# Performance work log

Hardware: AMD Instinct MI355X
Metric: run time of the kernel (lower is better)

## Reference

```python
import jax, jax.numpy as jnp
import numpy as np

SEQ = 2048
D_MODEL = 2048
N_HEAD = 16
D_QK = 128
D_V = 128


def setup_inputs() -> dict:
    key = jax.random.key(0)
    ks = jax.random.split(key, 5)
    return {
        "x": jax.random.normal(ks[0], (SEQ, D_MODEL), dtype=jnp.float32),
        "q": jax.random.normal(ks[1], (N_HEAD, D_MODEL, D_QK), dtype=jnp.float32),
        "k": jax.random.normal(ks[2], (N_HEAD, D_MODEL, D_QK), dtype=jnp.float32),
        "v": jax.random.normal(ks[3], (N_HEAD, D_MODEL, D_V), dtype=jnp.float32),
        "o": jax.random.normal(ks[4], (N_HEAD, D_V, D_MODEL), dtype=jnp.float32),
        "theta_factor": jnp.asarray(10000.0, dtype=jnp.float32),
    }


def _rope_embed(x, theta_factor, d_qk):
    # x: [n_head, seq, d_qk]; faithful to source: rate is LINEAR in theta_factor
    seq = x.shape[1]
    d_rope = d_qk // 2
    rate = theta_factor * (-jnp.arange(d_rope, dtype=x.dtype) / d_rope)  # [d_rope]
    pos = jnp.arange(seq, dtype=x.dtype)                                 # [seq]
    rot = pos[:, None] * rate[None, :]                                   # [seq, d_rope]
    sin, cos = jnp.sin(rot), jnp.cos(rot)
    x1, x2 = x[..., :d_rope], x[..., d_rope:]
    y = jnp.concatenate([cos * x1 - sin * x2, sin * x1 + cos * x2], axis=-1)
    return y / d_qk ** 0.25  # qk_layer_norm is None path


def reference(x, q, k, v, o, theta_factor):
    seq, d_model = x.shape
    n_head, _, d_qk = q.shape
    d_v = v.shape[2]
    scale = 1.0 / jnp.sqrt(jnp.asarray(n_head * d_v * d_model, dtype=x.dtype))
    # causal mask: (tril - 1) * 1e9, as in source
    mask = (jnp.tril(jnp.ones((seq, seq), dtype=x.dtype)) - 1.0) * 1e9
    # per-head projections (vmapped heads expressed as einsum over h)
    rq = _rope_embed(jnp.einsum('sd,hde->hse', x, q), theta_factor, d_qk)
    rk = _rope_embed(jnp.einsum('sd,hde->hse', x, k), theta_factor, d_qk)
    vs = jnp.einsum('sd,hdv->hsv', x, v)
    scores = jnp.einsum('hse,hte->hst', rq, rk) + mask  # [h, s, s]
    w = jax.nn.softmax(scores, axis=-1)
    y = jnp.einsum('hst,htv->hsv', w, vs)
    z = jnp.einsum('hsv,hvd->sd', y, o)
    return z * scale
```

## Files before the change

kernel.cpp:

```cpp
#include <hip/hip_runtime.h>
#include <math.h>


typedef _Float16 half_t;
typedef __attribute__((ext_vector_type(8))) _Float16 half8;
typedef __attribute__((ext_vector_type(4))) float f32x4;

#define SEQ   2048
#define DM    2048
#define NHEAD 16

__device__ __forceinline__ f32x4 mfma16(half8 a, half8 b, f32x4 c) {
  return __builtin_amdgcn_mfma_f32_16x16x32_f16(a, b, c, 0, 0, 0);
}

__device__ __forceinline__ void gll16(const half_t* g, half_t* l) {
  __builtin_amdgcn_global_load_lds(
      (const __attribute__((address_space(1))) unsigned int*)g,
      (__attribute__((address_space(3))) unsigned int*)l, 16, 0, 0);
}

template <int CTRL>
__device__ __forceinline__ float dppf(float v) {
  int r = __builtin_amdgcn_mov_dpp(__builtin_bit_cast(int, v), CTRL, 0xF, 0xF,
                                   true);
  return __builtin_bit_cast(float, r);
}
__device__ __forceinline__ float red16_max(float v) {
  v = fmaxf(v, dppf<0xB1>(v));
  v = fmaxf(v, dppf<0x4E>(v));
  v = fmaxf(v, dppf<0x141>(v));
  v = fmaxf(v, dppf<0x140>(v));
  return v;
}
__device__ __forceinline__ float red16_sum(float v) {
  v += dppf<0xB1>(v);
  v += dppf<0x4E>(v);
  v += dppf<0x141>(v);
  v += dppf<0x140>(v);
  return v;
}

__global__ __launch_bounds__(256)
void k_split4(const float* __restrict__ in, half_t* __restrict__ hi,
              half_t* __restrict__ lo, int n4) {
  int i = blockIdx.x * 256 + threadIdx.x;
  if (i >= n4) return;
  float4 v = ((const float4*)in)[i];
  union { half_t h[4]; uint2 u; } H, L;
  H.h[0] = (half_t)v.x; H.h[1] = (half_t)v.y;
  H.h[2] = (half_t)v.z; H.h[3] = (half_t)v.w;
  L.h[0] = (half_t)(v.x - (float)H.h[0]);
  L.h[1] = (half_t)(v.y - (float)H.h[1]);
  L.h[2] = (half_t)(v.z - (float)H.h[2]);
  L.h[3] = (half_t)(v.w - (float)H.h[3]);
  *(uint2*)&hi[(size_t)i * 4] = H.u;
  *(uint2*)&lo[(size_t)i * 4] = L.u;
}

__global__ __launch_bounds__(256)
void k_transpose(const float* __restrict__ in, half_t* __restrict__ hi,
                 half_t* __restrict__ lo, int R, int C) {
  __shared__ float tile[32][33];
  size_t bo = (size_t)blockIdx.z * R * C;
  int c0 = blockIdx.x * 32, r0 = blockIdx.y * 32;
  int tx = threadIdx.x & 31, ty = threadIdx.x >> 5;
#pragma unroll
  for (int i = 0; i < 32; i += 8)
    tile[ty + i][tx] = in[bo + (size_t)(r0 + ty + i) * C + c0 + tx];
  __syncthreads();
#pragma unroll
  for (int i = 0; i < 32; i += 8) {
    float v = tile[tx][ty + i];
    half_t h = (half_t)v;
    size_t oidx = bo + (size_t)(c0 + ty + i) * R + r0 + tx;
    hi[oidx] = h;
    if (lo) lo[oidx] = (half_t)(v - (float)h);
  }
}


__global__ __launch_bounds__(256, 2)
void k_proj(const half_t* __restrict__ Xh, const half_t* __restrict__ Xl,
            const half_t* __restrict__ WTh, const half_t* __restrict__ WTl,
            float* __restrict__ Craw) {
  __shared__ __align__(16) half_t sAh[128 * 64], sAl[128 * 64];
  __shared__ __align__(16) half_t sBh[128 * 64], sBl[128 * 64];
  int y = blockIdx.y;
  int m0 = blockIdx.x * 128;
  const half_t* wth = WTh + (size_t)y * 128 * DM;
  const half_t* wtl = WTl + (size_t)y * 128 * DM;
  int lane = threadIdx.x & 63, wave = threadIdx.x >> 6;
  int l15 = lane & 15, quad = lane >> 4;
  int wm = wave >> 1, wn = wave & 1;

  f32x4 acc[4][4];
#pragma unroll
  for (int a = 0; a < 4; ++a)
#pragma unroll
    for (int b = 0; b < 4; ++b) acc[a][b] = (f32x4)0.0f;

  for (int kt = 0; kt < DM / 64; ++kt) {
    int k0 = kt * 64;
#pragma unroll
    for (int i = 0; i < 4; ++i) {
      int c = wave * 4 + i;
      int g = c * 64 + lane;
      int row = g >> 3;
      int lc = (g & 7) ^ (row & 7);
      size_t ro = (size_t)row * DM + k0 + lc * 8;
      gll16(Xh + (size_t)m0 * DM + ro, sAh + c * 512);
      gll16(Xl + (size_t)m0 * DM + ro, sAl + c * 512);
      gll16(wth + ro, sBh + c * 512);
      gll16(wtl + ro, sBl + c * 512);
    }
    __syncthreads();
#pragma unroll
    for (int kk = 0; kk < 2; ++kk) {
      half8 ah[4], al[4], bh[4], bl[4];
#pragma unroll
      for (int t = 0; t < 4; ++t) {
        int ar = wm * 64 + t * 16 + l15;
        int br = wn * 64 + t * 16 + l15;
        int ao = ar * 64 + (((kk * 4 + quad) ^ (ar & 7)) * 8);
        int bo = br * 64 + (((kk * 4 + quad) ^ (br & 7)) * 8);
        ah[t] = *(const half8*)&sAh[ao];
        al[t] = *(const half8*)&sAl[ao];
        bh[t] = *(const half8*)&sBh[bo];
        bl[t] = *(const half8*)&sBl[bo];
      }
#pragma unroll
      for (int im = 0; im < 4; ++im)
#pragma unroll
        for (int in = 0; in < 4; ++in) {
          acc[im][in] = mfma16(ah[im], bh[in], acc[im][in]);
          acc[im][in] = mfma16(ah[im], bl[in], acc[im][in]);
          acc[im][in] = mfma16(al[im], bh[in], acc[im][in]);
        }
    }
    __syncthreads();
  }
  float* cb = Craw + (size_t)y * SEQ * 128;
#pragma unroll
  for (int im = 0; im < 4; ++im)
#pragma unroll
    for (int in = 0; in < 4; ++in)
#pragma unroll
      for (int r = 0; r < 4; ++r) {
        int row = m0 + wm * 64 + im * 16 + quad * 4 + r;
        int col = wn * 64 + in * 16 + l15;
        cb[(size_t)row * 128 + col] = acc[im][in][r];
      }
}

__global__ __launch_bounds__(256)
void k_rope(const float* __restrict__ Craw, half_t* __restrict__ Rh,
            half_t* __restrict__ Rl, const float* __restrict__ thetap) {
  int e = threadIdx.x & 63, sl = threadIdx.x >> 6;
  int s = blockIdx.x * 4 + sl;
  float th = thetap[0];
  float rate = th * (-(float)e * (1.0f / 64.0f));
  float rot = (float)s * rate;
  double rev = (double)rot * 0.15915494309189535;
  double fr = rev - rint(rev);
  float thr = (float)(fr * 6.283185307179586);
  float sn = sinf(thr), cs = cosf(thr);
  const float inv4 = 0.2973017787506803f;
  float csn = cs * inv4, snn = sn * inv4;
#pragma unroll 4
  for (int y = 0; y < 32; ++y) {
    size_t base = ((size_t)y * SEQ + s) * 128;
    float x1 = Craw[base + e];
    float x2 = Craw[base + 64 + e];
    float y1 = csn * x1 - snn * x2;
    float y2 = snn * x1 + csn * x2;
    half_t h1 = (half_t)y1, h2 = (half_t)y2;
    Rh[base + e] = h1;       Rl[base + e] = (half_t)(y1 - (float)h1);
    Rh[base + 64 + e] = h2;  Rl[base + 64 + e] = (half_t)(y2 - (float)h2);
  }
}

template <int HALF_OUT>
__global__ __launch_bounds__(256)
void k_gemm1(const half_t* __restrict__ A, const half_t* __restrict__ B,
             void* __restrict__ Cv, float scale) {
  __shared__ __align__(16) half_t sA[128 * 64], sB[128 * 64];
  int am0 = blockIdx.y * 128, bn0 = blockIdx.x * 128;
  int lane = threadIdx.x & 63, wave = threadIdx.x >> 6;
  int l15 = lane & 15, quad = lane >> 4;
  int wm = wave >> 1, wn = wave & 1;

  f32x4 acc[4][4];
#pragma unroll
  for (int a = 0; a < 4; ++a)
#pragma unroll
    for (int b = 0; b < 4; ++b) acc[a][b] = (f32x4)0.0f;

  for (int kt = 0; kt < DM / 64; ++kt) {
    int k0 = kt * 64;
#pragma unroll
    for (int i = 0; i < 4; ++i) {
      int c = wave * 4 + i;
      int g = c * 64 + lane;
      int row = g >> 3;
      int lc = (g & 7) ^ (row & 7);
      size_t ro = (size_t)row * 2048 + k0 + lc * 8;
      gll16(A + (size_t)am0 * 2048 + ro, sA + c * 512);
      gll16(B + (size_t)bn0 * 2048 + ro, sB + c * 512);
    }
    __syncthreads();
#pragma unroll
    for (int kk = 0; kk < 2; ++kk) {
      half8 ah[4], bh[4];
#pragma unroll
      for (int t = 0; t < 4; ++t) {
        int ar = wm * 64 + t * 16 + l15;
        int br = wn * 64 + t * 16 + l15;
        ah[t] = *(const half8*)&sA[ar * 64 + (((kk * 4 + quad) ^ (ar & 7)) * 8)];
        bh[t] = *(const half8*)&sB[br * 64 + (((kk * 4 + quad) ^ (br & 7)) * 8)];
      }
#pragma unroll
      for (int im = 0; im < 4; ++im)
#pragma unroll
        for (int in = 0; in < 4; ++in)
          acc[im][in] = mfma16(ah[im], bh[in], acc[im][in]);
    }
    __syncthreads();
  }
#pragma unroll
  for (int im = 0; im < 4; ++im)
#pragma unroll
    for (int in = 0; in < 4; ++in)
#pragma unroll
      for (int r = 0; r < 4; ++r) {
        int row = am0 + wm * 64 + im * 16 + quad * 4 + r;
        int col = bn0 + wn * 64 + in * 16 + l15;
        if (HALF_OUT)
          ((half_t*)Cv)[(size_t)row * 2048 + col] = (half_t)(acc[im][in][r] * scale);
        else
          ((float*)Cv)[(size_t)row * 2048 + col] = acc[im][in][r] * scale;
      }
}

__global__ __launch_bounds__(256, 2)
void k_flash(const half_t* __restrict__ Rh, const half_t* __restrict__ Rl,
             const half_t* __restrict__ VST, half_t* __restrict__ Ybig) {
  int idx = blockIdx.x;
  int h = idx & 15;
  int qt = (idx < 256) ? (31 - (idx >> 4)) : ((idx - 256) >> 4);
  int lane = threadIdx.x & 63, wave = threadIdx.x >> 6;
  int l15 = lane & 15, quad = lane >> 4;

  const half_t* RQh = Rh + (size_t)h * SEQ * 128;
  const half_t* RQl = Rl + (size_t)h * SEQ * 128;
  const half_t* RKh = Rh + (size_t)(NHEAD + h) * SEQ * 128;
  const half_t* RKl = Rl + (size_t)(NHEAD + h) * SEQ * 128;
  const half_t* Vt  = VST + (size_t)h * 128 * SEQ;

  __shared__ __align__(16) half_t sKh[64 * 128];
  __shared__ __align__(16) half_t sKl[64 * 128];
  __shared__ __align__(16) half_t sVt[128 * 64];
  __shared__ __align__(16) half_t sP[64 * 72];

  int q0 = qt * 64;

  half8 qh[4], ql[4];
#pragma unroll
  for (int kk = 0; kk < 4; ++kk) {
    size_t ad = (size_t)(q0 + wave * 16 + l15) * 128 + kk * 32 + quad * 8;
    qh[kk] = *(const half8*)&RQh[ad];
    ql[kk] = *(const half8*)&RQl[ad];
  }

  float m_st[4], l_st[4];
  f32x4 oacc[8];
#pragma unroll
  for (int r = 0; r < 4; ++r) { m_st[r] = -INFINITY; l_st[r] = 0.0f; }
#pragma unroll
  for (int iv = 0; iv < 8; ++iv) oacc[iv] = (f32x4)0.0f;

  int nkb = qt + 1;
  for (int kb = 0; kb < nkb; ++kb) {
    int t0 = kb * 64;
#pragma unroll
    for (int i = 0; i < 4; ++i) {
      int c = wave * 4 + i;
      int rk = c * 4 + (lane >> 4);
      int ck = (lane & 15) ^ (rk & 15);
      gll16(RKh + (size_t)(t0 + rk) * 128 + ck * 8, sKh + c * 512);
      gll16(RKl + (size_t)(t0 + rk) * 128 + ck * 8, sKl + c * 512);
      int rv = c * 8 + (lane >> 3);
      int cv = (lane & 7) ^ (rv & 7);
      gll16(Vt + (size_t)rv * SEQ + t0 + cv * 8, sVt + c * 512);
    }
    __syncthreads();

    f32x4 sacc[4];
#pragma unroll
    for (int in = 0; in < 4; ++in) sacc[in] = (f32x4)0.0f;
#pragma unroll
    for (int kk = 0; kk < 4; ++kk)
#pragma unroll
      for (int in = 0; in < 4; ++in) {
        int bo = (in * 16 + l15) * 128 + (((kk * 4 + quad) ^ l15) * 8);
        half8 bh = *(const half8*)&sKh[bo];
        half8 bl = *(const half8*)&sKl[bo];
        sacc[in] = mfma16(qh[kk], bh, sacc[in]);
        sacc[in] = mfma16(qh[kk], bl, sacc[in]);
        sacc[in] = mfma16(ql[kk], bh, sacc[in]);
      }
    if (kb == qt) {
#pragma unroll
      for (int in = 0; in < 4; ++in)
#pragma unroll
        for (int r = 0; r < 4; ++r)
          if (in * 16 + l15 > wave * 16 + quad * 4 + r) sacc[in][r] = -1e30f;
    }
    float alpha[4];
#pragma unroll
    for (int r = 0; r < 4; ++r) {
      float mx = fmaxf(fmaxf(sacc[0][r], sacc[1][r]),
                       fmaxf(sacc[2][r], sacc[3][r]));
      mx = red16_max(mx);
      float mnew = fmaxf(m_st[r], mx);
      alpha[r] = __expf(m_st[r] - mnew);
      float sum = 0.0f;
#pragma unroll
      for (int in = 0; in < 4; ++in) {
        float p = __expf(sacc[in][r] - mnew);
        sacc[in][r] = p;
        sum += p;
      }
      sum = red16_sum(sum);
      l_st[r] = l_st[r] * alpha[r] + sum;
      m_st[r] = mnew;
    }
#pragma unroll
    for (int in = 0; in < 4; ++in)
#pragma unroll
      for (int r = 0; r < 4; ++r)
        sP[(wave * 16 + quad * 4 + r) * 72 + in * 16 + l15] =
            (half_t)sacc[in][r];
#pragma unroll
    for (int iv = 0; iv < 8; ++iv)
#pragma unroll
      for (int r = 0; r < 4; ++r) oacc[iv][r] *= alpha[r];

#pragma unroll
    for (int kk2 = 0; kk2 < 2; ++kk2) {
      half8 pa =
          *(const half8*)&sP[(wave * 16 + l15) * 72 + kk2 * 32 + quad * 8];
#pragma unroll
      for (int iv = 0; iv < 8; ++iv) {
        half8 vb = *(const half8*)&sVt[(iv * 16 + l15) * 64 +
                                       (((kk2 * 4 + quad) ^ (l15 & 7)) * 8)];
        oacc[iv] = mfma16(pa, vb, oacc[iv]);
      }
    }
    __syncthreads();
  }
  float invl[4];
#pragma unroll
  for (int r = 0; r < 4; ++r) invl[r] = 1.0f / l_st[r];
#pragma unroll
  for (int iv = 0; iv < 8; ++iv)
#pragma unroll
    for (int r = 0; r < 4; ++r) {
      int row = q0 + wave * 16 + quad * 4 + r;
      int col = h * 128 + iv * 16 + l15;
      Ybig[(size_t)row * 2048 + col] = (half_t)(oacc[iv][r] * invl[r]);
    }
}

extern "C" void kernel_launch(void* const* d_in, const int* in_sizes, int n_in,
                              void* d_out, int out_size, void* d_ws,
                              size_t ws_size, hipStream_t stream) {
  const float* x = (const float*)d_in[0];
  const float* q = (const float*)d_in[1];
  const float* k = (const float*)d_in[2];
  const float* v = (const float*)d_in[3];
  const float* o = (const float*)d_in[4];
  const float* theta = (const float*)d_in[5];
  float* out = (float*)d_out;

  char* ws = (char*)d_ws;
  const size_t HB = (size_t)2048 * 2048 * 2;
  half_t* Xh  = (half_t*)(ws);
  half_t* Xl  = (half_t*)(ws + HB);
  half_t* WTh = (half_t*)(ws + 2 * HB);
  half_t* WTl = (half_t*)(ws + 4 * HB);
  half_t* VhT = (half_t*)(ws + 6 * HB);
  half_t* OT  = (half_t*)(ws + 7 * HB);
  float*  Craw = (float*)(ws + 8 * HB);
  half_t* Rh = WTh;
  half_t* Rl = WTl;
  half_t* VST  = (half_t*)(ws + 8 * HB);
  half_t* Ybig = (half_t*)(ws + 9 * HB);

  k_split4<<<4096, 256, 0, stream>>>(x, Xh, Xl, (2048 * 2048) / 4);
  k_transpose<<<dim3(4, 64, 16), 256, 0, stream>>>(q, WTh, WTl, 2048, 128);
  k_transpose<<<dim3(4, 64, 16), 256, 0, stream>>>(
      k, WTh + (size_t)16 * 128 * 2048, WTl + (size_t)16 * 128 * 2048, 2048, 128);
  k_transpose<<<dim3(4, 64, 16), 256, 0, stream>>>(v, VhT, nullptr, 2048, 128);
  k_transpose<<<dim3(64, 64, 1), 256, 0, stream>>>(o, OT, nullptr, 2048, 2048);
  k_proj<<<dim3(16, 32), 256, 0, stream>>>(Xh, Xl, WTh, WTl, Craw);
  k_rope<<<512, 256, 0, stream>>>(Craw, Rh, Rl, theta);
  k_gemm1<1><<<dim3(16, 16), 256, 0, stream>>>(VhT, Xh, VST, 1.0f);
  k_flash<<<512, 256, 0, stream>>>(Rh, Rl, VST, Ybig);
  k_gemm1<0><<<dim3(16, 16), 256, 0, stream>>>(Ybig, OT, out, 1.0f / 2048.0f);
}
```

Before: 380.9 us.

## Merge preprocessing kernels, fuse RoPE into projection epilogue, halve gemm M tile

Five preprocessing launches (split, four transposes) are merged into one k_pre kernel, which also precomputes a sin/cos table. RoPE moves into the k_proj epilogue: accumulators are staged through LDS and the rotated hi/lo fp16 results are written directly, so the fp32 Craw intermediate round trip and the separate rope launch go away. k_gemm1 switches to 64x128 tiles to double the block count for the V and output GEMMs. This trades more LDS traffic and extra barriers in the projection epilogue, plus a rearranged workspace, for less global memory traffic and launch overhead.

New measurement: 354.7 us. 6.9% less time.

```diff
diff --git a/kernel.cpp b/kernel.cpp
--- a/kernel.cpp
+++ b/kernel.cpp
@@ -41,51 +41,91 @@
   return v;
 }
 
-__global__ __launch_bounds__(256)
-void k_split4(const float* __restrict__ in, half_t* __restrict__ hi,
-              half_t* __restrict__ lo, int n4) {
-  int i = blockIdx.x * 256 + threadIdx.x;
-  if (i >= n4) return;
-  float4 v = ((const float4*)in)[i];
-  union { half_t h[4]; uint2 u; } H, L;
-  H.h[0] = (half_t)v.x; H.h[1] = (half_t)v.y;
-  H.h[2] = (half_t)v.z; H.h[3] = (half_t)v.w;
-  L.h[0] = (half_t)(v.x - (float)H.h[0]);
-  L.h[1] = (half_t)(v.y - (float)H.h[1]);
-  L.h[2] = (half_t)(v.z - (float)H.h[2]);
-  L.h[3] = (half_t)(v.w - (float)H.h[3]);
-  *(uint2*)&hi[(size_t)i * 4] = H.u;
-  *(uint2*)&lo[(size_t)i * 4] = L.u;
-}
-
-__global__ __launch_bounds__(256)
-void k_transpose(const float* __restrict__ in, half_t* __restrict__ hi,
-                 half_t* __restrict__ lo, int R, int C) {
-  __shared__ float tile[32][33];
-  size_t bo = (size_t)blockIdx.z * R * C;
-  int c0 = blockIdx.x * 32, r0 = blockIdx.y * 32;
-  int tx = threadIdx.x & 31, ty = threadIdx.x >> 5;
+__device__ __forceinline__ void tpose32(const float* __restrict__ in,
+                                        half_t* __restrict__ hi,
+                                        half_t* __restrict__ lo, int R, int C,
+                                        int r0, int c0, float (*tile)[33],
+                                        int tid) {
+  int tx = tid & 31, ty = tid >> 5;
 #pragma unroll
   for (int i = 0; i < 32; i += 8)
-    tile[ty + i][tx] = in[bo + (size_t)(r0 + ty + i) * C + c0 + tx];
+    tile[ty + i][tx] = in[(size_t)(r0 + ty + i) * C + c0 + tx];
   __syncthreads();
 #pragma unroll
   for (int i = 0; i < 32; i += 8) {
     float v = tile[tx][ty + i];
     half_t h = (half_t)v;
-    size_t oidx = bo + (size_t)(c0 + ty + i) * R + r0 + tx;
+    size_t oidx = (size_t)(c0 + ty + i) * R + r0 + tx;
     hi[oidx] = h;
     if (lo) lo[oidx] = (half_t)(v - (float)h);
   }
 }
 
+__global__ __launch_bounds__(256)
+void k_pre(const float* __restrict__ x, const float* __restrict__ q,
+           const float* __restrict__ k, const float* __restrict__ v,
+           const float* __restrict__ o, const float* __restrict__ thetap,
+           half_t* __restrict__ Xh, half_t* __restrict__ Xl,
+           half_t* __restrict__ WTh, half_t* __restrict__ WTl,
+           half_t* __restrict__ VhT, half_t* __restrict__ OT,
+           float2* __restrict__ trig) {
+  __shared__ float tile[32][33];
+  int b = blockIdx.x, tid = threadIdx.x;
+  if (b < 4096) {
+    int i = b * 256 + tid;
+    float4 vv = ((const float4*)x)[i];
+    union { half_t h[4]; uint2 u; } H, L;
+    H.h[0] = (half_t)vv.x; H.h[1] = (half_t)vv.y;
+    H.h[2] = (half_t)vv.z; H.h[3] = (half_t)vv.w;
+    L.h[0] = (half_t)(vv.x - (float)H.h[0]);
+    L.h[1] = (half_t)(vv.y - (float)H.h[1]);
+    L.h[2] = (half_t)(vv.z - (float)H.h[2]);
+    L.h[3] = (half_t)(vv.w - (float)H.h[3]);
+    *(uint2*)&Xh[(size_t)i * 4] = H.u;
+    *(uint2*)&Xl[(size_t)i * 4] = L.u;
+  } else if (b < 16384) {
+    int j = b - 4096;
+    int which = j >> 12, z = (j >> 8) & 15, tb = j & 255;
+    int c0 = (tb & 3) * 32, r0 = (tb >> 2) * 32;
+    const float* src =
+        (which == 0 ? q : which == 1 ? k : v) + (size_t)z * 2048 * 128;
+    size_t doff = (size_t)z * 128 * 2048;
+    if (which == 0)
+      tpose32(src, WTh + doff, WTl + doff, 2048, 128, r0, c0, tile, tid);
+    else if (which == 1) {
+      size_t koff = (size_t)16 * 128 * 2048 + doff;
+      tpose32(src, WTh + koff, WTl + koff, 2048, 128, r0, c0, tile, tid);
+    } else
+      tpose32(src, VhT + doff, nullptr, 2048, 128, r0, c0, tile, tid);
+  } else if (b < 20480) {
+    int j = b - 16384;
+    int c0 = (j & 63) * 32, r0 = (j >> 6) * 32;
+    tpose32(o, OT, nullptr, 2048, 2048, r0, c0, tile, tid);
+  } else {
+    int idx = (b - 20480) * 256 + tid;
+    int s = idx >> 6, e = idx & 63;
+    float th = thetap[0];
+    float rate = th * (-(float)e * (1.0f / 64.0f));
+    float rot = (float)s * rate;
+    double rev = (double)rot * 0.15915494309189535;
+    double fr = rev - rint(rev);
+    float thr = (float)(fr * 6.283185307179586);
+    float sn = sinf(thr), cs = cosf(thr);
+    const float inv4 = 0.2973017787506803f;
+    trig[idx] = make_float2(cs * inv4, sn * inv4);
+  }
+}
 
 __global__ __launch_bounds__(256, 2)
 void k_proj(const half_t* __restrict__ Xh, const half_t* __restrict__ Xl,
             const half_t* __restrict__ WTh, const half_t* __restrict__ WTl,
-            float* __restrict__ Craw) {
-  __shared__ __align__(16) half_t sAh[128 * 64], sAl[128 * 64];
-  __shared__ __align__(16) half_t sBh[128 * 64], sBl[128 * 64];
+            const float2* __restrict__ trig, half_t* __restrict__ Rh,
+            half_t* __restrict__ Rl) {
+  __shared__ __align__(16) char smem[65536];
+  half_t* sAh = (half_t*)smem;
+  half_t* sAl = (half_t*)(smem + 16384);
+  half_t* sBh = (half_t*)(smem + 32768);
+  half_t* sBl = (half_t*)(smem + 49152);
   int y = blockIdx.y;
   int m0 = blockIdx.x * 128;
   const half_t* wth = WTh + (size_t)y * 128 * DM;
@@ -140,43 +180,37 @@
     }
     __syncthreads();
   }
-  float* cb = Craw + (size_t)y * SEQ * 128;
-#pragma unroll
-  for (int im = 0; im < 4; ++im)
-#pragma unroll
-    for (int in = 0; in < 4; ++in)
-#pragma unroll
-      for (int r = 0; r < 4; ++r) {
-        int row = m0 + wm * 64 + im * 16 + quad * 4 + r;
-        int col = wn * 64 + in * 16 + l15;
-        cb[(size_t)row * 128 + col] = acc[im][in][r];
-      }
-}
-
-__global__ __launch_bounds__(256)
-void k_rope(const float* __restrict__ Craw, half_t* __restrict__ Rh,
-            half_t* __restrict__ Rl, const float* __restrict__ thetap) {
-  int e = threadIdx.x & 63, sl = threadIdx.x >> 6;
-  int s = blockIdx.x * 4 + sl;
-  float th = thetap[0];
-  float rate = th * (-(float)e * (1.0f / 64.0f));
-  float rot = (float)s * rate;
-  double rev = (double)rot * 0.15915494309189535;
-  double fr = rev - rint(rev);
-  float thr = (float)(fr * 6.283185307179586);
-  float sn = sinf(thr), cs = cosf(thr);
-  const float inv4 = 0.2973017787506803f;
-  float csn = cs * inv4, snn = sn * inv4;
+  float* tile = (float*)smem;
+  size_t ybase = (size_t)y * SEQ * 128;
+#pragma unroll
+  for (int p = 0; p < 2; ++p) {
+    if (p) __syncthreads();
+    if (wm == p) {
+#pragma unroll
+      for (int im = 0; im < 4; ++im)
+#pragma unroll
+        for (int in = 0; in < 4; ++in)
+#pragma unroll
+          for (int r = 0; r < 4; ++r)
+            tile[(im * 16 + quad * 4 + r) * 132 + wn * 64 + in * 16 + l15] =
+                acc[im][in][r];
+    }
+    __syncthreads();
+    int e = lane;
 #pragma unroll 4
-  for (int y = 0; y < 32; ++y) {
-    size_t base = ((size_t)y * SEQ + s) * 128;
-    float x1 = Craw[base + e];
-    float x2 = Craw[base + 64 + e];
-    float y1 = csn * x1 - snn * x2;
-    float y2 = snn * x1 + csn * x2;
-    half_t h1 = (half_t)y1, h2 = (half_t)y2;
-    Rh[base + e] = h1;       Rl[base + e] = (half_t)(y1 - (float)h1);
-    Rh[base + 64 + e] = h2;  Rl[base + 64 + e] = (half_t)(y2 - (float)h2);
+    for (int rr = 0; rr < 16; ++rr) {
+      int rloc = wave * 16 + rr;
+      int s = m0 + p * 64 + rloc;
+      float x1 = tile[rloc * 132 + e];
+      float x2 = tile[rloc * 132 + 64 + e];
+      float2 sc = trig[s * 64 + e];
+      float y1 = sc.x * x1 - sc.y * x2;
+      float y2 = sc.y * x1 + sc.x * x2;
+      half_t h1 = (half_t)y1, h2 = (half_t)y2;
+      size_t base = ybase + (size_t)s * 128;
+      Rh[base + e] = h1;       Rl[base + e] = (half_t)(y1 - (float)h1);
+      Rh[base + 64 + e] = h2;  Rl[base + 64 + e] = (half_t)(y2 - (float)h2);
+    }
   }
 }
 
@@ -184,43 +218,52 @@
 __global__ __launch_bounds__(256)
 void k_gemm1(const half_t* __restrict__ A, const half_t* __restrict__ B,
              void* __restrict__ Cv, float scale) {
-  __shared__ __align__(16) half_t sA[128 * 64], sB[128 * 64];
-  int am0 = blockIdx.y * 128, bn0 = blockIdx.x * 128;
+  __shared__ __align__(16) half_t sA[64 * 64], sB[128 * 64];
+  int am0 = blockIdx.y * 64, bn0 = blockIdx.x * 128;
   int lane = threadIdx.x & 63, wave = threadIdx.x >> 6;
   int l15 = lane & 15, quad = lane >> 4;
   int wm = wave >> 1, wn = wave & 1;
 
-  f32x4 acc[4][4];
-#pragma unroll
-  for (int a = 0; a < 4; ++a)
+  f32x4 acc[2][4];
+#pragma unroll
+  for (int a = 0; a < 2; ++a)
 #pragma unroll
     for (int b = 0; b < 4; ++b) acc[a][b] = (f32x4)0.0f;
 
   for (int kt = 0; kt < DM / 64; ++kt) {
     int k0 = kt * 64;
 #pragma unroll
-    for (int i = 0; i < 4; ++i) {
-      int c = wave * 4 + i;
-      int g = c * 64 + lane;
+    for (int i = 0; i < 2; ++i) {
+      int g0 = (i * 4 + wave) * 64;
+      int g = g0 + lane;
       int row = g >> 3;
       int lc = (g & 7) ^ (row & 7);
-      size_t ro = (size_t)row * 2048 + k0 + lc * 8;
-      gll16(A + (size_t)am0 * 2048 + ro, sA + c * 512);
-      gll16(B + (size_t)bn0 * 2048 + ro, sB + c * 512);
+      gll16(A + (size_t)(am0 + row) * 2048 + k0 + lc * 8, sA + g0 * 8);
+    }
+#pragma unroll
+    for (int i = 0; i < 4; ++i) {
+      int g0 = (i * 4 + wave) * 64;
+      int g = g0 + lane;
+      int row = g >> 3;
+      int lc = (g & 7) ^ (row & 7);
+      gll16(B + (size_t)(bn0 + row) * 2048 + k0 + lc * 8, sB + g0 * 8);
     }
     __syncthreads();
 #pragma unroll
     for (int kk = 0; kk < 2; ++kk) {
-      half8 ah[4], bh[4];
+      half8 ah[2], bh[4];
+#pragma unroll
+      for (int t = 0; t < 2; ++t) {
+        int ar = wm * 32 + t * 16 + l15;
+        ah[t] = *(const half8*)&sA[ar * 64 + (((kk * 4 + quad) ^ (ar & 7)) * 8)];
+      }
 #pragma unroll
       for (int t = 0; t < 4; ++t) {
-        int ar = wm * 64 + t * 16 + l15;
         int br = wn * 64 + t * 16 + l15;
-        ah[t] = *(const half8*)&sA[ar * 64 + (((kk * 4 + quad) ^ (ar & 7)) * 8)];
         bh[t] = *(const half8*)&sB[br * 64 + (((kk * 4 + quad) ^ (br & 7)) * 8)];
       }
 #pragma unroll
-      for (int im = 0; im < 4; ++im)
+      for (int im = 0; im < 2; ++im)
 #pragma unroll
         for (int in = 0; in < 4; ++in)
           acc[im][in] = mfma16(ah[im], bh[in], acc[im][in]);
@@ -228,12 +271,12 @@
     __syncthreads();
   }
 #pragma unroll
-  for (int im = 0; im < 4; ++im)
+  for (int im = 0; im < 2; ++im)
 #pragma unroll
     for (int in = 0; in < 4; ++in)
 #pragma unroll
       for (int r = 0; r < 4; ++r) {
-        int row = am0 + wm * 64 + im * 16 + quad * 4 + r;
+        int row = am0 + wm * 32 + im * 16 + quad * 4 + r;
         int col = bn0 + wn * 64 + in * 16 + l15;
         if (HALF_OUT)
           ((half_t*)Cv)[(size_t)row * 2048 + col] = (half_t)(acc[im][in][r] * scale);
@@ -385,27 +428,22 @@
 
   char* ws = (char*)d_ws;
   const size_t HB = (size_t)2048 * 2048 * 2;
-  half_t* Xh  = (half_t*)(ws);
-  half_t* Xl  = (half_t*)(ws + HB);
-  half_t* WTh = (half_t*)(ws + 2 * HB);
-  half_t* WTl = (half_t*)(ws + 4 * HB);
-  half_t* VhT = (half_t*)(ws + 6 * HB);
-  half_t* OT  = (half_t*)(ws + 7 * HB);
-  float*  Craw = (float*)(ws + 8 * HB);
-  half_t* Rh = WTh;
-  half_t* Rl = WTl;
-  half_t* VST  = (half_t*)(ws + 8 * HB);
-  half_t* Ybig = (half_t*)(ws + 9 * HB);
-
-  k_split4<<<4096, 256, 0, stream>>>(x, Xh, Xl, (2048 * 2048) / 4);
-  k_transpose<<<dim3(4, 64, 16), 256, 0, stream>>>(q, WTh, WTl, 2048, 128);
-  k_transpose<<<dim3(4, 64, 16), 256, 0, stream>>>(
-      k, WTh + (size_t)16 * 128 * 2048, WTl + (size_t)16 * 128 * 2048, 2048, 128);
-  k_transpose<<<dim3(4, 64, 16), 256, 0, stream>>>(v, VhT, nullptr, 2048, 128);
-  k_transpose<<<dim3(64, 64, 1), 256, 0, stream>>>(o, OT, nullptr, 2048, 2048);
-  k_proj<<<dim3(16, 32), 256, 0, stream>>>(Xh, Xl, WTh, WTl, Craw);
-  k_rope<<<512, 256, 0, stream>>>(Craw, Rh, Rl, theta);
-  k_gemm1<1><<<dim3(16, 16), 256, 0, stream>>>(VhT, Xh, VST, 1.0f);
+  half_t* Xh   = (half_t*)(ws);
+  half_t* Xl   = (half_t*)(ws + HB);
+  half_t* WTh  = (half_t*)(ws + 2 * HB);
+  half_t* WTl  = (half_t*)(ws + 4 * HB);
+  half_t* VhT  = (half_t*)(ws + 6 * HB);
+  half_t* OT   = (half_t*)(ws + 7 * HB);
+  half_t* Rh   = (half_t*)(ws + 8 * HB);
+  half_t* Rl   = (half_t*)(ws + 10 * HB);
+  float2* trig = (float2*)(ws + 12 * HB);
+  half_t* VST  = (half_t*)(ws + 2 * HB);
+  half_t* Ybig = (half_t*)(ws + 3 * HB);
+
+  k_pre<<<20992, 256, 0, stream>>>(x, q, k, v, o, theta, Xh, Xl, WTh, WTl,
+                                   VhT, OT, trig);
+  k_proj<<<dim3(16, 32), 256, 0, stream>>>(Xh, Xl, WTh, WTl, trig, Rh, Rl);
+  k_gemm1<1><<<dim3(16, 32), 256, 0, stream>>>(VhT, Xh, VST, 1.0f);
   k_flash<<<512, 256, 0, stream>>>(Rh, Rl, VST, Ybig);
-  k_gemm1<0><<<dim3(16, 16), 256, 0, stream>>>(Ybig, OT, out, 1.0f / 2048.0f);
-}
+  k_gemm1<0><<<dim3(16, 32), 256, 0, stream>>>(Ybig, OT, out, 1.0f / 2048.0f);
+}
```
